# Optimization experiments

Measured on AMD Instinct MI355X. Metric: run time of the kernel, lower is better.

Reference implementation:

```python
import jax, jax.numpy as jnp
import numpy as np

B, MN, GN, ME, GE = 1, 40962, 65160, 327660, 163848
MEMB = EEMB = 256
H1, H2 = 512, 64
EPS = 1e-5


def setup_inputs() -> dict:
    key = jax.random.key(0)
    ks = jax.random.split(key, 16)
    s = 0.05
    return {
        "gx": jax.random.normal(ks[0], (B, GN, MEMB), jnp.float32),
        "mx": jax.random.normal(ks[1], (B, MN, MEMB), jnp.float32),
        "me_i": jax.random.randint(ks[2], (2, ME), 0, MN),
        "me_x": jax.random.normal(ks[3], (B, ME, EEMB), jnp.float32),
        "g2me_i": jax.random.randint(ks[4], (2, GE), 0, MN),
        "g2me_x": jax.random.normal(ks[5], (B, GE, EEMB), jnp.float32),
        "m2ge_i": jax.random.randint(ks[6], (2, GE), 0, MN),
        "m2ge_x": jax.random.normal(ks[7], (B, GE, EEMB), jnp.float32),
        # learned params (Linear stored as [in, out]; y = x @ W + b, math-equivalent to torch)
        "W1": jax.random.normal(ks[8], (2 * MEMB + EEMB, H1), jnp.float32) * s,
        "b1": jnp.zeros((H1,), jnp.float32),
        "W2": jax.random.normal(ks[9], (H1, H2), jnp.float32) * s,
        "b2": jnp.zeros((H2,), jnp.float32),
        "W3": jax.random.normal(ks[10], (H2, EEMB), jnp.float32) * s,
        "b3": jnp.zeros((EEMB,), jnp.float32),
        # LayerNorm([m_enum, eemb]) -> elementwise affine over last two dims
        "ln_w": jnp.ones((ME, EEMB), jnp.float32),
        "ln_b": jnp.zeros((ME, EEMB), jnp.float32),
    }


def reference(gx, mx, me_i, me_x, g2me_i, g2me_x, m2ge_i, m2ge_x,
              W1, b1, W2, b2, W3, b3, ln_w, ln_b):
    row, col = me_i[0], me_i[1]
    # gather sender/receiver mesh-node features per edge: [B, ME, 2*MEMB+EEMB]
    h = jnp.concatenate([mx[:, row], mx[:, col], me_x], axis=-1)
    h = jax.nn.silu(h @ W1 + b1)
    h = jax.nn.silu(h @ W2 + b2)
    h = h @ W3 + b3
    # LayerNorm over the last TWO dims (m_enum, eemb), as nn.LayerNorm([m_enum, eemb])
    mean = jnp.mean(h, axis=(-2, -1), keepdims=True)
    var = jnp.var(h, axis=(-2, -1), keepdims=True)
    h = (h - mean) * jax.lax.rsqrt(var + EPS) * ln_w + ln_b
    me_x_new = me_x + h
    return (gx, mx, me_i, me_x_new, g2me_i, g2me_x, m2ge_i, m2ge_x)
```

## Files before the change

### kernel.cpp

```cpp
#include <hip/hip_runtime.h>
#include <hip/hip_bf16.h>

typedef unsigned short u16;
typedef unsigned int u32;
typedef __attribute__((ext_vector_type(8))) short bfrag8;
typedef __attribute__((ext_vector_type(4))) float f32x4;

#define ME_N 327660
#define MN_N 40962
#define MEMB_N 256
#define H1_N 512
#define H2_N 64
#define EEMB_N 256
#define LN_EPS 1e-5f
#define NBLK 5120

static __device__ __forceinline__ u16 f2bf(float f) {
  __hip_bfloat16 h = __float2bfloat16(f);
  return *reinterpret_cast<u16*>(&h);
}
static __device__ __forceinline__ float bf2f(u16 u) {
  union { u32 i; float f; } x; x.i = ((u32)u) << 16; return x.f;
}
static __device__ __forceinline__ u32 pack2(float a, float b) {
  return (u32)f2bf(a) | ((u32)f2bf(b) << 16);
}
static __device__ __forceinline__ float silu_f(float x) {
  return x / (1.0f + __expf(-x));
}
static __device__ __forceinline__ void gload_lds16(const void* g, void* l) {
  __builtin_amdgcn_global_load_lds(
      (const __attribute__((address_space(1))) void*)g,
      (__attribute__((address_space(3))) void*)l, 16, 0, 0);
}

__global__ void i2f_kernel(const int* __restrict__ src, float* __restrict__ dst, int n) {
  int i = blockIdx.x * 256 + threadIdx.x;
  if (i < n) dst[i] = (float)src[i];
}

__global__ void bfconv_kernel(const float* __restrict__ src, u16* __restrict__ dst, int n) {
  int i = (blockIdx.x * 256 + threadIdx.x) * 8;
  if (i >= n) return;
  float4 v0 = reinterpret_cast<const float4*>(src + i)[0];
  float4 v1 = reinterpret_cast<const float4*>(src + i)[1];
  uint4 q;
  q.x = pack2(v0.x, v0.y); q.y = pack2(v0.z, v0.w);
  q.z = pack2(v1.x, v1.y); q.w = pack2(v1.z, v1.w);
  *reinterpret_cast<uint4*>(dst + i) = q;
}

__global__ void wconv1_kernel(const float* __restrict__ src, u16* __restrict__ dst) {
  int i = blockIdx.x * 256 + threadIdx.x;
  if (i >= 512 * 768) return;
  int e   = i & 7;
  int l16 = (i >> 3) & 15;
  int k4  = (i >> 7) & 3;
  int ks  = (i >> 9) & 1;
  int rest = i >> 10;
  int kc = rest % 12;
  int J  = rest / 12;
  int n = J * 16 + l16;
  int k = kc * 64 + ks * 32 + k4 * 8 + e;
  dst[i] = f2bf(src[(size_t)k * 512 + n]);
}

__global__ void wconv_kernel(const float* __restrict__ src, u16* __restrict__ dst,
                             int K, int N) {
  int i = blockIdx.x * 256 + threadIdx.x;
  if (i >= K * N) return;
  int n = i / K;
  int k = i - n * K;
  dst[i] = f2bf(src[(size_t)k * N + n]);
}

__launch_bounds__(1024, 4)
__global__ void gemm_fused_kernel(const u16* __restrict__ mxb, const int* __restrict__ me_i,
                                  const float* __restrict__ me_x,
                                  const u16* __restrict__ w1f, const float* __restrict__ b1,
                                  const u16* __restrict__ w2t, const float* __restrict__ b2,
                                  const u16* __restrict__ w3t, const float* __restrict__ b3,
                                  u16* __restrict__ h3, float* __restrict__ partials) {
  __shared__ u16 S[16384];
  __shared__ float red[32];

  const int t = threadIdx.x;
  const int m0 = blockIdx.x * 64;
  const int lane = t & 63;
  const int w = t >> 6;
  const int l16 = lane & 15;
  const int k4 = lane >> 4;
  const int h7 = l16 & 7;

  const int r_st = (t >> 3) & 63;
  const int g_st = t & 7;
  const int gsw = (g_st ^ (r_st & 7)) * 8;
  const int mg = min(m0 + r_st, ME_N - 1);
  const u16* rowr = mxb + (size_t)me_i[mg] * MEMB_N;
  const u16* rowc = mxb + (size_t)me_i[ME_N + mg] * MEMB_N;

  const int r4 = t >> 4;
  const int sub = t & 15;
  const int sgrp = sub >> 1, shalf = sub & 1;
  const int mg4 = min(m0 + r4, ME_N - 1);
  const float* pef = me_x + (size_t)mg4 * EEMB_N + ((sgrp ^ (r4 & 7)) * 8 + shalf * 4);
  const int doff = r4 * 64 + sgrp * 8 + shalf * 4;

  const f32x4 zero = {0.f, 0.f, 0.f, 0.f};
  f32x4 acc[2][4];
#pragma unroll
  for (int jj = 0; jj < 2; ++jj)
#pragma unroll
    for (int i = 0; i < 4; ++i) acc[jj][i] = zero;

  auto stage_dma = [&](int kcn) {
    if (w < 8) {
      const u16* src = (kcn < 4 ? rowr : rowc) + (kcn & 3) * 64 + gsw;
      gload_lds16(src, S + (kcn & 1) * 4096 + w * 512);
    }
  };
  auto loadB = [&](int kc, bfrag8 (&bfr)[2][2]) {
    const u16* wbase = w1f + (size_t)(w * 2) * 12288 + (size_t)kc * 1024 + k4 * 128 + l16 * 8;
#pragma unroll
    for (int ks = 0; ks < 2; ++ks)
#pragma unroll
      for (int jj = 0; jj < 2; ++jj)
        bfr[ks][jj] = *reinterpret_cast<const bfrag8*>(wbase + (size_t)jj * 12288 + ks * 512);
  };
  auto compute = [&](int kc, const bfrag8 (&bfr)[2][2]) {
    const u16* ab = S + (kc & 1) * 4096;
#pragma unroll
    for (int ks = 0; ks < 2; ++ks) {
      bfrag8 a[4];
#pragma unroll
      for (int i = 0; i < 4; ++i)
        a[i] = *reinterpret_cast<const bfrag8*>(
            &ab[(i * 16 + l16) * 64 + (((ks * 4 + k4) ^ h7) * 8)]);
#pragma unroll
      for (int jj = 0; jj < 2; ++jj)
#pragma unroll
        for (int i = 0; i < 4; ++i)
          acc[jj][i] = __builtin_amdgcn_mfma_f32_16x16x32_bf16(bfr[ks][jj], a[i], acc[jj][i], 0, 0, 0);
    }
  };
  auto packA = [&](const float4& fq, int slot) {
    uint2 pq = make_uint2(pack2(fq.x, fq.y), pack2(fq.z, fq.w));
    *reinterpret_cast<uint2*>(S + slot * 4096 + doff) = pq;
  };
  auto waitv = [&]() {
    if (w < 8) { asm volatile("s_waitcnt vmcnt(5)" ::: "memory"); }
    else       { asm volatile("s_waitcnt vmcnt(4)" ::: "memory"); }
  };

  bfrag8 B0[2][2], B1[2][2];
  float4 fq;

  stage_dma(0);
  loadB(0, B0);
#pragma unroll
  for (int kcp = 0; kcp < 6; kcp += 2) {
    loadB(kcp + 1, B1);
    stage_dma(kcp + 1);
    waitv();
    __builtin_amdgcn_s_barrier();
    compute(kcp, B0);
    __builtin_amdgcn_s_barrier();
    loadB(kcp + 2, B0);
    stage_dma(kcp + 2);
    waitv();
    __builtin_amdgcn_s_barrier();
    compute(kcp + 1, B1);
    __builtin_amdgcn_s_barrier();
  }
  {
    loadB(7, B1);
    stage_dma(7);
    waitv();
    __builtin_amdgcn_s_barrier();
    compute(6, B0);
    __builtin_amdgcn_s_barrier();
  }
  {
    fq = *reinterpret_cast<const float4*>(pef);
    loadB(8, B0);
    asm volatile("s_waitcnt vmcnt(5)" ::: "memory");
    __builtin_amdgcn_s_barrier();
    compute(7, B1);
    packA(fq, 0);
    asm volatile("s_waitcnt lgkmcnt(0)" ::: "memory");
    __builtin_amdgcn_s_barrier();
  }
  {
    fq = *reinterpret_cast<const float4*>(pef + 64);
    loadB(9, B1);
    compute(8, B0);
    packA(fq, 1);
    asm volatile("s_waitcnt lgkmcnt(0)" ::: "memory");
    __builtin_amdgcn_s_barrier();
  }
  {
    fq = *reinterpret_cast<const float4*>(pef + 128);
    loadB(10, B0);
    compute(9, B1);
    packA(fq, 0);
    asm volatile("s_waitcnt lgkmcnt(0)" ::: "memory");
    __builtin_amdgcn_s_barrier();
  }
  {
    fq = *reinterpret_cast<const float4*>(pef + 192);
    loadB(11, B1);
    compute(10, B0);
    packA(fq, 1);
    asm volatile("s_waitcnt lgkmcnt(0)" ::: "memory");
    __builtin_amdgcn_s_barrier();
  }
  {
    compute(11, B1);
  }
  __syncthreads();

  const int kh = w >> 3;
  const int n2s = w & 3;
  const int ihalf = (w >> 2) & 1;
  const int n2 = n2s * 16 + l16;

  f32x4 acc2p[2];
#pragma unroll
  for (int ii = 0; ii < 2; ++ii) acc2p[ii] = zero;

#pragma unroll
  for (int h = 0; h < 2; ++h) {
    if (kh == h) {
#pragma unroll
      for (int jj = 0; jj < 2; ++jj) {
        const int colbase = (w & 7) * 32 + jj * 16 + k4 * 4;
        const float4 bq = *reinterpret_cast<const float4*>(b1 + h * 256 + colbase);
        const int grp = colbase >> 3, off = colbase & 7;
#pragma unroll
        for (int i = 0; i < 4; ++i) {
          float x0 = silu_f(acc[jj][i][0] + bq.x);
          float x1 = silu_f(acc[jj][i][1] + bq.y);
          float x2 = silu_f(acc[jj][i][2] + bq.z);
          float x3 = silu_f(acc[jj][i][3] + bq.w);
          uint2 pq = make_uint2(pack2(x0, x1), pack2(x2, x3));
          *reinterpret_cast<uint2*>(&S[(i * 16 + l16) * 256 + ((grp ^ h7) * 8 + off)]) = pq;
        }
      }
    }
    __syncthreads();
    if (kh == h) {
#pragma unroll
      for (int ksl = 0; ksl < 8; ++ksl) {
        bfrag8 w2f = *reinterpret_cast<const bfrag8*>(
            w2t + (size_t)n2 * 512 + h * 256 + ksl * 32 + k4 * 8);
#pragma unroll
        for (int ii = 0; ii < 2; ++ii) {
          const int i = ihalf * 2 + ii;
          bfrag8 a2 = *reinterpret_cast<const bfrag8*>(
              &S[(i * 16 + l16) * 256 + (((ksl * 4 + k4) ^ h7) * 8)]);
          acc2p[ii] = __builtin_amdgcn_mfma_f32_16x16x32_bf16(w2f, a2, acc2p[ii], 0, 0, 0);
        }
      }
    }
    __syncthreads();
  }

  float* LDSf = reinterpret_cast<float*>(S);
  u16* h2T = S + 12288;
  if (kh == 1) {
#pragma unroll
    for (int ii = 0; ii < 2; ++ii)
      *reinterpret_cast<f32x4*>(
          &LDSf[(((n2s * 2 + ihalf) * 2 + ii) * 64 + lane) * 4]) = acc2p[ii];
  }
  __syncthreads();
  if (kh == 0) {
    const float4 b2q = *reinterpret_cast<const float4*>(b2 + n2s * 16 + k4 * 4);
    const int grpn = n2s * 2 + (k4 >> 1), offn = (k4 & 1) * 4;
#pragma unroll
    for (int ii = 0; ii < 2; ++ii) {
      const int i = ihalf * 2 + ii;
      f32x4 o = *reinterpret_cast<f32x4*>(
          &LDSf[(((n2s * 2 + ihalf) * 2 + ii) * 64 + lane) * 4]);
      float x0 = silu_f(acc2p[ii][0] + o[0] + b2q.x);
      float x1 = silu_f(acc2p[ii][1] + o[1] + b2q.y);
      float x2 = silu_f(acc2p[ii][2] + o[2] + b2q.z);
      float x3 = silu_f(acc2p[ii][3] + o[3] + b2q.w);
      uint2 pq = make_uint2(pack2(x0, x1), pack2(x2, x3));
      *reinterpret_cast<uint2*>(&h2T[(i * 16 + l16) * 64 + ((grpn ^ h7) * 8 + offn)]) = pq;
    }
  }
  __syncthreads();

  bfrag8 a3[2][4];
#pragma unroll
  for (int ks = 0; ks < 2; ++ks)
#pragma unroll
    for (int i = 0; i < 4; ++i)
      a3[ks][i] = *reinterpret_cast<const bfrag8*>(
          &h2T[(i * 16 + l16) * 64 + (((ks * 4 + k4) ^ h7) * 8)]);
  bfrag8 w3f[2];
#pragma unroll
  for (int ks = 0; ks < 2; ++ks)
    w3f[ks] = *reinterpret_cast<const bfrag8*>(
        w3t + (size_t)(w * 16 + l16) * 64 + ks * 32 + k4 * 8);
  __syncthreads();

  f32x4 acc3[4];
#pragma unroll
  for (int i = 0; i < 4; ++i) acc3[i] = zero;
#pragma unroll
  for (int ks = 0; ks < 2; ++ks)
#pragma unroll
    for (int i = 0; i < 4; ++i)
      acc3[i] = __builtin_amdgcn_mfma_f32_16x16x32_bf16(w3f[ks], a3[ks][i], acc3[i], 0, 0, 0);

  float lsum = 0.f, lsq = 0.f;
  {
    const float4 b3q = *reinterpret_cast<const float4*>(b3 + w * 16 + k4 * 4);
    const int grp3 = w * 2 + (k4 >> 1), off3 = (k4 & 1) * 4;
#pragma unroll
    for (int i = 0; i < 4; ++i) {
      float x0 = acc3[i][0] + b3q.x;
      float x1 = acc3[i][1] + b3q.y;
      float x2 = acc3[i][2] + b3q.z;
      float x3 = acc3[i][3] + b3q.w;
      if (m0 + i * 16 + l16 < ME_N) {
        lsum += (x0 + x1) + (x2 + x3);
        lsq += x0 * x0 + x1 * x1 + x2 * x2 + x3 * x3;
      }
      uint2 pq = make_uint2(pack2(x0, x1), pack2(x2, x3));
      *reinterpret_cast<uint2*>(&S[(i * 16 + l16) * 256 + ((grp3 ^ h7) * 8 + off3)]) = pq;
    }
  }
#pragma unroll
  for (int o = 32; o > 0; o >>= 1) {
    lsum += __shfl_down(lsum, o, 64);
    lsq  += __shfl_down(lsq, o, 64);
  }
  if (lane == 0) { red[w] = lsum; red[16 + w] = lsq; }
  __syncthreads();

  {
    u16* dst = h3 + (size_t)(m0 + r4) * EEMB_N;
#pragma unroll
    for (int q = 0; q < 2; ++q) {
      const int G = sub * 2 + q;
      uint4 v = *reinterpret_cast<const uint4*>(&S[r4 * 256 + ((G ^ (r4 & 7)) * 8)]);
      *reinterpret_cast<uint4*>(dst + G * 8) = v;
    }
  }
  if (t == 0) {
    float s1 = 0.f, s2 = 0.f;
#pragma unroll
    for (int q = 0; q < 16; ++q) { s1 += red[q]; s2 += red[16 + q]; }
    partials[2 * blockIdx.x] = s1;
    partials[2 * blockIdx.x + 1] = s2;
  }
}

__global__ void reduce_kernel(const float* __restrict__ partials, int n,
                              float* __restrict__ stats) {
  __shared__ float s1[256], s2[256];
  float a = 0.f, b = 0.f;
  for (int i = threadIdx.x; i < n; i += 256) { a += partials[2 * i]; b += partials[2 * i + 1]; }
  s1[threadIdx.x] = a; s2[threadIdx.x] = b;
  __syncthreads();
  for (int off = 128; off > 0; off >>= 1) {
    if ((int)threadIdx.x < off) {
      s1[threadIdx.x] += s1[threadIdx.x + off];
      s2[threadIdx.x] += s2[threadIdx.x + off];
    }
    __syncthreads();
  }
  if (threadIdx.x == 0) {
    double cnt = (double)ME_N * (double)EEMB_N;
    double mean = (double)s1[0] / cnt;
    double var = (double)s2[0] / cnt - mean * mean;
    stats[0] = (float)mean;
    stats[1] = (float)(1.0 / sqrt(var + (double)LN_EPS));
  }
}

__launch_bounds__(256)
__global__ void final_kernel(const u16* __restrict__ h3, const float* __restrict__ me_x,
                             const float* __restrict__ ln_w, const float* __restrict__ ln_b,
                             const float* __restrict__ stats, float* __restrict__ out) {
  const size_t total = (size_t)ME_N * EEMB_N;
  size_t i = ((size_t)blockIdx.x * 256 + threadIdx.x) * 8;
  if (i >= total) return;
  const float mean = stats[0], inv = stats[1];
  uint4 hv = *reinterpret_cast<const uint4*>(h3 + i);
  float h[8];
  h[0] = bf2f((u16)(hv.x & 0xffff)); h[1] = bf2f((u16)(hv.x >> 16));
  h[2] = bf2f((u16)(hv.y & 0xffff)); h[3] = bf2f((u16)(hv.y >> 16));
  h[4] = bf2f((u16)(hv.z & 0xffff)); h[5] = bf2f((u16)(hv.z >> 16));
  h[6] = bf2f((u16)(hv.w & 0xffff)); h[7] = bf2f((u16)(hv.w >> 16));
  float4 m0 = reinterpret_cast<const float4*>(me_x + i)[0];
  float4 m1 = reinterpret_cast<const float4*>(me_x + i)[1];
  float4 w0 = reinterpret_cast<const float4*>(ln_w + i)[0];
  float4 w1 = reinterpret_cast<const float4*>(ln_w + i)[1];
  float4 c0 = reinterpret_cast<const float4*>(ln_b + i)[0];
  float4 c1 = reinterpret_cast<const float4*>(ln_b + i)[1];
  float4 o0, o1;
  o0.x = m0.x + (h[0] - mean) * inv * w0.x + c0.x;
  o0.y = m0.y + (h[1] - mean) * inv * w0.y + c0.y;
  o0.z = m0.z + (h[2] - mean) * inv * w0.z + c0.z;
  o0.w = m0.w + (h[3] - mean) * inv * w0.w + c0.w;
  o1.x = m1.x + (h[4] - mean) * inv * w1.x + c1.x;
  o1.y = m1.y + (h[5] - mean) * inv * w1.y + c1.y;
  o1.z = m1.z + (h[6] - mean) * inv * w1.z + c1.z;
  o1.w = m1.w + (h[7] - mean) * inv * w1.w + c1.w;
  reinterpret_cast<float4*>(out + i)[0] = o0;
  reinterpret_cast<float4*>(out + i)[1] = o1;
}

extern "C" void kernel_launch(void* const* d_in, const int* in_sizes, int n_in,
                              void* d_out, int out_size, void* d_ws, size_t ws_size,
                              hipStream_t stream) {
  const float* mx   = (const float*)d_in[1];
  const int*   me_i = (const int*)d_in[2];
  const float* me_x = (const float*)d_in[3];
  const float* W1 = (const float*)d_in[8];
  const float* b1 = (const float*)d_in[9];
  const float* W2 = (const float*)d_in[10];
  const float* b2 = (const float*)d_in[11];
  const float* W3 = (const float*)d_in[12];
  const float* b3 = (const float*)d_in[13];
  const float* ln_w = (const float*)d_in[14];
  const float* ln_b = (const float*)d_in[15];

  char* ws = (char*)d_ws;
  u16* w1f = (u16*)(ws + 0);
  u16* w2t = (u16*)(ws + 786432);
  u16* w3t = (u16*)(ws + 851968);
  u16* mxb = (u16*)(ws + 884736);
  u16* h3  = (u16*)(ws + 21857280);
  float* partials = (float*)(ws + 189629440);
  float* stats    = (float*)(ws + 189670400);

  size_t off[8]; size_t a = 0;
  for (int i = 0; i < 8; ++i) { off[i] = a; a += (size_t)in_sizes[i]; }

  for (int i = 0; i < 8; ++i) {
    if (i == 3) continue;
    if (i == 2 || i == 4 || i == 6) {
      int n = in_sizes[i];
      i2f_kernel<<<(n + 255) / 256, 256, 0, stream>>>(
          (const int*)d_in[i], (float*)d_out + off[i], n);
    } else {
      hipMemcpyAsync((char*)d_out + off[i] * 4, d_in[i], (size_t)in_sizes[i] * 4,
                     hipMemcpyDeviceToDevice, stream);
    }
  }

  wconv1_kernel<<<(512 * 768 + 255) / 256, 256, 0, stream>>>(W1, w1f);
  wconv_kernel<<<(512 * 64 + 255) / 256, 256, 0, stream>>>(W2, w2t, 512, 64);
  wconv_kernel<<<(64 * 256 + 255) / 256, 256, 0, stream>>>(W3, w3t, 64, 256);
  {
    int n = MN_N * MEMB_N;
    bfconv_kernel<<<(n / 8 + 255) / 256, 256, 0, stream>>>(mx, mxb, n);
  }

  gemm_fused_kernel<<<NBLK, 1024, 0, stream>>>(mxb, me_i, me_x, w1f, b1, w2t, b2,
                                               w3t, b3, h3, partials);
  reduce_kernel<<<1, 256, 0, stream>>>(partials, NBLK, stats);

  const size_t total8 = (size_t)ME_N * EEMB_N / 8;
  final_kernel<<<(int)((total8 + 255) / 256), 256, 0, stream>>>(
      h3, me_x, ln_w, ln_b, stats, (float*)d_out + off[3]);
}
```

Before: 1.034 ms.

## Deepen first-layer A-tile pipeline to four LDS slots with one barrier per step

The first GEMM's gathered A-tile staging grows from a double buffer to a four-slot LDS ring. DMA for chunk k+3 is issued while chunk k is computed, and each K-step now uses one barrier instead of two. The four me_x float4 loads are issued earlier into separate registers so their latency is hidden across several compute steps. This aims to cut barrier stalls and exposed gather latency, at the cost of more LDS (four slots) and extra registers, which may reduce occupancy.

After: 1.011 ms. 2.3% less time.

```diff
diff --git a/kernel.cpp b/kernel.cpp
--- a/kernel.cpp
+++ b/kernel.cpp
@@ -116,7 +116,7 @@
   auto stage_dma = [&](int kcn) {
     if (w < 8) {
       const u16* src = (kcn < 4 ? rowr : rowc) + (kcn & 3) * 64 + gsw;
-      gload_lds16(src, S + (kcn & 1) * 4096 + w * 512);
+      gload_lds16(src, S + (kcn & 3) * 4096 + w * 512);
     }
   };
   auto loadB = [&](int kc, bfrag8 (&bfr)[2][2]) {
@@ -128,7 +128,7 @@
         bfr[ks][jj] = *reinterpret_cast<const bfrag8*>(wbase + (size_t)jj * 12288 + ks * 512);
   };
   auto compute = [&](int kc, const bfrag8 (&bfr)[2][2]) {
-    const u16* ab = S + (kc & 1) * 4096;
+    const u16* ab = S + (kc & 3) * 4096;
 #pragma unroll
     for (int ks = 0; ks < 2; ++ks) {
       bfrag8 a[4];
@@ -147,76 +147,53 @@
     uint2 pq = make_uint2(pack2(fq.x, fq.y), pack2(fq.z, fq.w));
     *reinterpret_cast<uint2*>(S + slot * 4096 + doff) = pq;
   };
-  auto waitv = [&]() {
-    if (w < 8) { asm volatile("s_waitcnt vmcnt(5)" ::: "memory"); }
-    else       { asm volatile("s_waitcnt vmcnt(4)" ::: "memory"); }
-  };
+
+#define WAITDMA() if (w < 8) { asm volatile("s_waitcnt vmcnt(10)" ::: "memory"); }
+#define BAR() __builtin_amdgcn_s_barrier(); asm volatile("" ::: "memory")
+#define LGKM0() asm volatile("s_waitcnt lgkmcnt(0)" ::: "memory")
 
   bfrag8 B0[2][2], B1[2][2];
-  float4 fq;
+  float4 fqA, fqB, fqC, fqD;
 
   stage_dma(0);
+  asm volatile("s_waitcnt vmcnt(63)" ::: "memory");
+  stage_dma(1);
+  asm volatile("s_waitcnt vmcnt(63)" ::: "memory");
+  stage_dma(2);
   loadB(0, B0);
-#pragma unroll
-  for (int kcp = 0; kcp < 6; kcp += 2) {
-    loadB(kcp + 1, B1);
-    stage_dma(kcp + 1);
-    waitv();
-    __builtin_amdgcn_s_barrier();
-    compute(kcp, B0);
-    __builtin_amdgcn_s_barrier();
-    loadB(kcp + 2, B0);
-    stage_dma(kcp + 2);
-    waitv();
-    __builtin_amdgcn_s_barrier();
-    compute(kcp + 1, B1);
-    __builtin_amdgcn_s_barrier();
-  }
-  {
-    loadB(7, B1);
-    stage_dma(7);
-    waitv();
-    __builtin_amdgcn_s_barrier();
-    compute(6, B0);
-    __builtin_amdgcn_s_barrier();
-  }
-  {
-    fq = *reinterpret_cast<const float4*>(pef);
-    loadB(8, B0);
-    asm volatile("s_waitcnt vmcnt(5)" ::: "memory");
-    __builtin_amdgcn_s_barrier();
-    compute(7, B1);
-    packA(fq, 0);
-    asm volatile("s_waitcnt lgkmcnt(0)" ::: "memory");
-    __builtin_amdgcn_s_barrier();
-  }
-  {
-    fq = *reinterpret_cast<const float4*>(pef + 64);
-    loadB(9, B1);
-    compute(8, B0);
-    packA(fq, 1);
-    asm volatile("s_waitcnt lgkmcnt(0)" ::: "memory");
-    __builtin_amdgcn_s_barrier();
-  }
-  {
-    fq = *reinterpret_cast<const float4*>(pef + 128);
-    loadB(10, B0);
-    compute(9, B1);
-    packA(fq, 0);
-    asm volatile("s_waitcnt lgkmcnt(0)" ::: "memory");
-    __builtin_amdgcn_s_barrier();
-  }
-  {
-    fq = *reinterpret_cast<const float4*>(pef + 192);
-    loadB(11, B1);
-    compute(10, B0);
-    packA(fq, 1);
-    asm volatile("s_waitcnt lgkmcnt(0)" ::: "memory");
-    __builtin_amdgcn_s_barrier();
-  }
-  {
-    compute(11, B1);
-  }
+
+  loadB(1, B1); WAITDMA(); BAR(); stage_dma(3); compute(0, B0);
+  loadB(2, B0); WAITDMA(); BAR(); stage_dma(4); compute(1, B1);
+  loadB(3, B1); WAITDMA(); BAR(); stage_dma(5); compute(2, B0);
+  loadB(4, B0); WAITDMA(); BAR(); stage_dma(6); compute(3, B1);
+  loadB(5, B1); WAITDMA(); BAR(); stage_dma(7); compute(4, B0);
+  loadB(6, B0); WAITDMA(); BAR();
+  fqA = *reinterpret_cast<const float4*>(pef);
+  compute(5, B1);
+  loadB(7, B1); WAITDMA(); BAR();
+  fqB = *reinterpret_cast<const float4*>(pef + 64);
+  compute(6, B0);
+  loadB(8, B0); WAITDMA(); BAR();
+  fqC = *reinterpret_cast<const float4*>(pef + 128);
+  compute(7, B1);
+  packA(fqA, 0); LGKM0();
+  loadB(9, B1); BAR();
+  fqD = *reinterpret_cast<const float4*>(pef + 192);
+  compute(8, B0);
+  packA(fqB, 1); LGKM0();
+  loadB(10, B0); BAR();
+  compute(9, B1);
+  packA(fqC, 2); LGKM0();
+  loadB(11, B1); BAR();
+  compute(10, B0);
+  packA(fqD, 3); LGKM0();
+  BAR();
+  compute(11, B1);
+
+#undef WAITDMA
+#undef BAR
+#undef LGKM0
+
   __syncthreads();
 
   const int kh = w >> 3;
```
